# Performance work log

Hardware: AMD Instinct MI355X
Metric: run time of the kernel (lower is better)

The kernel has to match this reference:

```python
import jax, jax.numpy as jnp
from jax import lax
import numpy as np

DIM = 384
HEADS = 8
MLP_HIDDEN = int(DIM * 4.0)
EPS = 1e-5


def layer_norm(x, g, b):
    m = jnp.mean(x, axis=-1, keepdims=True)
    v = jnp.mean((x - m) ** 2, axis=-1, keepdims=True)
    return (x - m) * lax.rsqrt(v + EPS) * g + b


def conv_pos_enc(x, H, W, w, b):
    # x: (B, N, C) -> depthwise 3x3 conv residual, act=Identity (cpe_act=False)
    B, N, C = x.shape
    feat = jnp.transpose(x, (0, 2, 1)).reshape(B, C, H, W)
    feat = lax.conv_general_dilated(
        feat, w, window_strides=(1, 1), padding='SAME',
        feature_group_count=C, dimension_numbers=('NCHW', 'OIHW', 'NCHW'))
    feat = feat + b[None, :, None, None]
    feat = jnp.transpose(feat.reshape(B, C, N), (0, 2, 1))
    return x + feat


def channel_attn(x, qkv_w, proj_w, proj_b):
    B, N, C = x.shape
    h = HEADS
    hd = C // h
    scale = hd ** (-0.5)
    qkv = x @ qkv_w.T                                # (B, N, 3C)
    qkv = qkv.reshape(B, N, 3, h, hd)
    qkv = jnp.transpose(qkv, (2, 0, 3, 1, 4))        # (3, B, h, N, hd)
    q, k, v = qkv[0], qkv[1], qkv[2]
    k = k * scale
    attn = jnp.einsum('bhnd,bhne->bhde', k, v)       # (B, h, hd, hd)
    attn = jax.nn.softmax(attn, axis=-1)
    out = jnp.einsum('bhde,bhne->bhnd', attn, q)     # (B, h, N, hd)
    out = jnp.transpose(out, (0, 2, 1, 3)).reshape(B, N, C)
    return out @ proj_w.T + proj_b


def mlp(x, fc1_w, fc1_b, fc2_w, fc2_b):
    h = jax.nn.gelu(x @ fc1_w.T + fc1_b, approximate=False)
    return h @ fc2_w.T + fc2_b


def setup_inputs() -> dict:
    key = jax.random.key(0)
    ks = jax.random.split(key, 12)
    C, Hd = DIM, MLP_HIDDEN
    s = 0.02
    return {
        'x': jax.random.normal(ks[0], (32, 784, C), dtype=jnp.float32),
        'H': 28,
        'W': 28,
        'cpe0_w': jax.random.normal(ks[1], (C, 1, 3, 3), dtype=jnp.float32) * s,
        'cpe0_b': jnp.zeros((C,), dtype=jnp.float32),
        'cpe1_w': jax.random.normal(ks[2], (C, 1, 3, 3), dtype=jnp.float32) * s,
        'cpe1_b': jnp.zeros((C,), dtype=jnp.float32),
        'norm1_g': jnp.ones((C,), dtype=jnp.float32),
        'norm1_b': jnp.zeros((C,), dtype=jnp.float32),
        'qkv_w': jax.random.normal(ks[3], (3 * C, C), dtype=jnp.float32) * s,
        'proj_w': jax.random.normal(ks[4], (C, C), dtype=jnp.float32) * s,
        'proj_b': jnp.zeros((C,), dtype=jnp.float32),
        'norm2_g': jnp.ones((C,), dtype=jnp.float32),
        'norm2_b': jnp.zeros((C,), dtype=jnp.float32),
        'fc1_w': jax.random.normal(ks[5], (Hd, C), dtype=jnp.float32) * s,
        'fc1_b': jnp.zeros((Hd,), dtype=jnp.float32),
        'fc2_w': jax.random.normal(ks[6], (C, Hd), dtype=jnp.float32) * s,
        'fc2_b': jnp.zeros((C,), dtype=jnp.float32),
    }


def reference(x, H, W, cpe0_w, cpe0_b, cpe1_w, cpe1_b, norm1_g, norm1_b,
              qkv_w, proj_w, proj_b, norm2_g, norm2_b,
              fc1_w, fc1_b, fc2_w, fc2_b):
    x = conv_pos_enc(x, H, W, cpe0_w, cpe0_b)
    cur = layer_norm(x, norm1_g, norm1_b)
    x = x + channel_attn(cur, qkv_w, proj_w, proj_b)
    x = conv_pos_enc(x, H, W, cpe1_w, cpe1_b)
    x = x + mlp(layer_norm(x, norm2_g, norm2_b), fc1_w, fc1_b, fc2_w, fc2_b)
    return x
```

## Files before the change

kernel.cpp:

```cpp
#include <hip/hip_runtime.h>
#include <hip/hip_bf16.h>
#include <math.h>
#include <stdint.h>

#define B_     32
#define HH_    28
#define WW_    28
#define N_     784
#define C_     384
#define M_     25088
#define HEADS_ 8
#define HD_    48
#define HID_   1536

typedef __bf16 bf16;
typedef __attribute__((ext_vector_type(8))) __bf16 bf16x8;
typedef __attribute__((ext_vector_type(4))) __bf16 bf16x4;
typedef __attribute__((ext_vector_type(4))) float f32x4;

__device__ __forceinline__ void gload_lds16(const void* g, void* l) {
    __builtin_amdgcn_global_load_lds(
        (const __attribute__((address_space(1))) unsigned int*)g,
        (__attribute__((address_space(3))) unsigned int*)(uintptr_t)l,
        16, 0, 0);
}

__global__ void convert4_kernel(const float* __restrict__ a, int na,
                                const float* __restrict__ b, int nb,
                                const float* __restrict__ c, int nc,
                                const float* __restrict__ d, int nd,
                                bf16* __restrict__ out) {
    int i = blockIdx.x * 256 + threadIdx.x;
    int j = i;
    const float* src;
    if (j < na) src = a + j;
    else { j -= na;
        if (j < nb) src = b + j;
        else { j -= nb;
            if (j < nc) src = c + j;
            else { j -= nc;
                if (j >= nd) return;
                src = d + j; } } }
    out[i] = (bf16)(*src);
}

__global__ __launch_bounds__(384)
void cpe_ln_kernel(const float* __restrict__ x, const float* __restrict__ w,
                   const float* __restrict__ bias, float* __restrict__ y,
                   const float* __restrict__ g, const float* __restrict__ beta,
                   bf16* __restrict__ lnout) {
    __shared__ float red[4][96];
    const int t = threadIdx.x;
    const int tpos = t / 96;
    const int cg = t - tpos * 96;
    const int c4 = cg * 4;
    const int row = blockIdx.x * 4 + tpos;
    const int b = row / N_;
    const int n = row - b * N_;
    const int py = n / WW_, px = n - py * WW_;
    const float* wc = w + c4 * 9;

    float4 acc = *(const float4*)(bias + c4);
    float4 ctr = *(const float4*)(x + (size_t)row * C_ + c4);

    if (py >= 1 && py <= 26 && px >= 1 && px <= 26) {
        const float* p0 = x + (size_t)(row - WW_ - 1) * C_ + c4;
        const float* p1 = p0 + (size_t)WW_ * C_;
        const float* p2 = p1 + (size_t)WW_ * C_;
        float4 a0 = *(const float4*)(p0);
        float4 a1 = *(const float4*)(p0 + C_);
        float4 a2 = *(const float4*)(p0 + 2 * C_);
        float4 b0 = *(const float4*)(p1);
        float4 b2 = *(const float4*)(p1 + 2 * C_);
        float4 c0 = *(const float4*)(p2);
        float4 c1 = *(const float4*)(p2 + C_);
        float4 c2 = *(const float4*)(p2 + 2 * C_);
        float4 b1 = ctr;
        #define TAP(V, TI) \
            acc.x += wc[TI] * V.x; acc.y += wc[9 + TI] * V.y; \
            acc.z += wc[18 + TI] * V.z; acc.w += wc[27 + TI] * V.w;
        TAP(a0, 0) TAP(a1, 1) TAP(a2, 2)
        TAP(b0, 3) TAP(b1, 4) TAP(b2, 5)
        TAP(c0, 6) TAP(c1, 7) TAP(c2, 8)
        #undef TAP
    } else {
        #pragma unroll
        for (int ky = 0; ky < 3; ky++) {
            int yy = py + ky - 1;
            if (yy < 0 || yy >= HH_) continue;
            #pragma unroll
            for (int kx = 0; kx < 3; kx++) {
                int xx = px + kx - 1;
                if (xx < 0 || xx >= WW_) continue;
                int tap = ky * 3 + kx;
                float4 xv = (ky == 1 && kx == 1) ? ctr
                          : *(const float4*)(x + (size_t)(b * N_ + yy * WW_ + xx) * C_ + c4);
                acc.x += wc[tap] * xv.x;
                acc.y += wc[9 + tap] * xv.y;
                acc.z += wc[18 + tap] * xv.z;
                acc.w += wc[27 + tap] * xv.w;
            }
        }
    }
    acc.x += ctr.x; acc.y += ctr.y; acc.z += ctr.z; acc.w += ctr.w;
    *(float4*)(y + (size_t)row * C_ + c4) = acc;

    red[tpos][cg] = acc.x + acc.y + acc.z + acc.w;
    __syncthreads();
    #pragma unroll
    for (int s = 48; s >= 3; s >>= 1) {
        if (cg < s) red[tpos][cg] += red[tpos][cg + s];
        __syncthreads();
    }
    float mean = (red[tpos][0] + red[tpos][1] + red[tpos][2]) * (1.f / C_);
    __syncthreads();
    float dx = acc.x - mean, dy = acc.y - mean, dz = acc.z - mean, dw = acc.w - mean;
    red[tpos][cg] = dx * dx + dy * dy + dz * dz + dw * dw;
    __syncthreads();
    #pragma unroll
    for (int s = 48; s >= 3; s >>= 1) {
        if (cg < s) red[tpos][cg] += red[tpos][cg + s];
        __syncthreads();
    }
    float var = (red[tpos][0] + red[tpos][1] + red[tpos][2]) * (1.f / C_);
    float rstd = rsqrtf(var + 1e-5f);
    float4 gv = *(const float4*)(g + c4);
    float4 bv = *(const float4*)(beta + c4);
    bf16x4 ov;
    ov[0] = (bf16)(dx * rstd * gv.x + bv.x);
    ov[1] = (bf16)(dy * rstd * gv.y + bv.y);
    ov[2] = (bf16)(dz * rstd * gv.z + bv.z);
    ov[3] = (bf16)(dw * rstd * gv.w + bv.w);
    *(bf16x4*)(lnout + (size_t)row * C_ + c4) = ov;
}

template<bool BIAS, bool GELU, bool RESID, bool OUTBF>
__global__ __launch_bounds__(256)
void gemm_kernel(const bf16* __restrict__ A, const bf16* __restrict__ Wt,
                 const float* __restrict__ bias, const float* __restrict__ resid,
                 void* __restrict__ outp, int M, int N, int K) {
    __shared__ __align__(16) bf16 As[2 * 128 * 32];
    __shared__ __align__(16) bf16 Bs[2 * 128 * 32];
    const int bm = blockIdx.y * 128, bn = blockIdx.x * 128;
    const int t = threadIdx.x;
    const int wave = t >> 6, lane = t & 63;
    const int wm = (wave & 1) * 64, wn = (wave >> 1) * 64;
    const int quad = lane >> 4, r = lane & 15;

    const int ldrow = lane >> 2;
    const int ldcol = (lane & 3) * 8;
    const bf16* ga0 = A  + (size_t)(bm + wave * 32 + ldrow) * K + ldcol;
    const bf16* ga1 = ga0 + (size_t)16 * K;
    const bf16* gb0 = Wt + (size_t)(bn + wave * 32 + ldrow) * K + ldcol;
    const bf16* gb1 = gb0 + (size_t)16 * K;
    const int lbase = wave * 32 * 32;

    f32x4 acc[4][4] = {};

    gload_lds16(ga0, &As[lbase]);
    gload_lds16(ga1, &As[lbase + 512]);
    gload_lds16(gb0, &Bs[lbase]);
    gload_lds16(gb1, &Bs[lbase + 512]);

    int buf = 0;
    for (int k0 = 0; k0 < K; k0 += 32) {
        __syncthreads();
        if (k0 + 32 < K) {
            const int nb = (buf ^ 1) * 4096;
            gload_lds16(ga0 + k0 + 32, &As[nb + lbase]);
            gload_lds16(ga1 + k0 + 32, &As[nb + lbase + 512]);
            gload_lds16(gb0 + k0 + 32, &Bs[nb + lbase]);
            gload_lds16(gb1 + k0 + 32, &Bs[nb + lbase + 512]);
        }
        const bf16* as = &As[buf * 4096];
        const bf16* bs = &Bs[buf * 4096];
        bf16x8 af[4], bfr[4];
        #pragma unroll
        for (int i = 0; i < 4; i++)
            af[i] = *(const bf16x8*)(&as[(wm + i * 16 + r) * 32 + quad * 8]);
        #pragma unroll
        for (int j = 0; j < 4; j++)
            bfr[j] = *(const bf16x8*)(&bs[(wn + j * 16 + r) * 32 + quad * 8]);
        #pragma unroll
        for (int i = 0; i < 4; i++)
            #pragma unroll
            for (int j = 0; j < 4; j++)
                acc[i][j] = __builtin_amdgcn_mfma_f32_16x16x32_bf16(af[i], bfr[j], acc[i][j], 0, 0, 0);
        buf ^= 1;
    }

    #pragma unroll
    for (int i = 0; i < 4; i++) {
        #pragma unroll
        for (int j = 0; j < 4; j++) {
            int n = bn + wn + j * 16 + r;
            float bv = BIAS ? bias[n] : 0.f;
            #pragma unroll
            for (int e = 0; e < 4; e++) {
                int m = bm + wm + i * 16 + quad * 4 + e;
                float val = acc[i][j][e] + bv;
                if (GELU) val = 0.5f * val * (1.f + erff(val * 0.70710678118654752f));
                if (RESID) val += resid[(size_t)m * N + n];
                if (OUTBF) ((bf16*)outp)[(size_t)m * N + n] = (bf16)val;
                else       ((float*)outp)[(size_t)m * N + n] = val;
            }
        }
    }
}

__global__ __launch_bounds__(256)
void attn_fused_kernel(const bf16* __restrict__ qkvb, bf16* __restrict__ outp) {
    __shared__ __align__(16) bf16 stage[4][3872];
    __shared__ float Sred[4][48][49];
    __shared__ __align__(16) bf16 attn_s[48 * 72];

    const int bh = blockIdx.x;
    const int b = bh >> 3, h = bh & 7;
    const int t = threadIdx.x;
    const int wave = t >> 6, lane = t & 63;
    const int quad = lane >> 4, r = lane & 15;
    const int tensor = lane >> 5;
    const int n_local = lane & 31;

    const size_t qkv_base = (size_t)b * N_ * 1152;
    const int toff = 384 + tensor * 384 + h * 48;

    f32x4 acc[3][3] = {};
    bf16* kT = &stage[wave][0];
    bf16* vT = &stage[wave][1936];
    bf16* myT = &stage[wave][tensor * 1936];

    for (int c = wave; c < 25; c += 4) {
        int n0 = c * 32;
        bf16 rowbuf[48];
        if (n0 + n_local < N_) {
            const uint4* src = (const uint4*)(qkvb + qkv_base + (size_t)(n0 + n_local) * 1152 + toff);
            #pragma unroll
            for (int i = 0; i < 6; i++) *(uint4*)(&rowbuf[i * 8]) = src[i];
        } else {
            #pragma unroll
            for (int i = 0; i < 48; i++) rowbuf[i] = (bf16)0.f;
        }
        #pragma unroll
        for (int d = 0; d < 48; d++) myT[d * 40 + n_local] = rowbuf[d];
        bf16x8 af[3], bfv[3];
        #pragma unroll
        for (int i = 0; i < 3; i++) af[i]  = *(const bf16x8*)(&kT[(i * 16 + r) * 40 + quad * 8]);
        #pragma unroll
        for (int j = 0; j < 3; j++) bfv[j] = *(const bf16x8*)(&vT[(j * 16 + r) * 40 + quad * 8]);
        #pragma unroll
        for (int i = 0; i < 3; i++)
            #pragma unroll
            for (int j = 0; j < 3; j++)
                acc[i][j] = __builtin_amdgcn_mfma_f32_16x16x32_bf16(af[i], bfv[j], acc[i][j], 0, 0, 0);
    }

    #pragma unroll
    for (int i = 0; i < 3; i++)
        #pragma unroll
        for (int j = 0; j < 3; j++)
            #pragma unroll
            for (int e = 0; e < 4; e++)
                Sred[wave][i * 16 + quad * 4 + e][j * 16 + r] = acc[i][j][e];
    __syncthreads();

    if (t < 48) {
        float row[48];
        float mx = -1e30f;
        #pragma unroll
        for (int e = 0; e < 48; e++) {
            float s = Sred[0][t][e] + Sred[1][t][e] + Sred[2][t][e] + Sred[3][t][e];
            s *= 0.14433756729740644f;
            row[e] = s;
            mx = fmaxf(mx, s);
        }
        float sum = 0.f;
        #pragma unroll
        for (int e = 0; e < 48; e++) { float ex = __expf(row[e] - mx); row[e] = ex; sum += ex; }
        float inv = 1.f / sum;
        #pragma unroll
        for (int e = 0; e < 48; e++) attn_s[t * 72 + e] = (bf16)(row[e] * inv);
        #pragma unroll
        for (int e = 48; e < 64; e++) attn_s[t * 72 + e] = (bf16)0.f;
    }
    __syncthreads();

    const bf16* qbase = qkvb + qkv_base + h * 48;
    for (int nt = wave; nt < 49; nt += 4) {
        int n0 = nt * 16;
        f32x4 oacc[3] = {};
        #pragma unroll
        for (int kc = 0; kc < 2; kc++) {
            bf16x8 bq = *(const bf16x8*)(qbase + (size_t)(n0 + r) * 1152 + kc * 32 + quad * 8);
            #pragma unroll
            for (int i = 0; i < 3; i++) {
                bf16x8 aa = *(const bf16x8*)(&attn_s[(i * 16 + r) * 72 + kc * 32 + quad * 8]);
                oacc[i] = __builtin_amdgcn_mfma_f32_16x16x32_bf16(aa, bq, oacc[i], 0, 0, 0);
            }
        }
        #pragma unroll
        for (int i = 0; i < 3; i++) {
            bf16x4 ov;
            #pragma unroll
            for (int e = 0; e < 4; e++) ov[e] = (bf16)oacc[i][e];
            *(bf16x4*)(outp + (size_t)(b * N_ + n0 + r) * 384 + h * 48 + i * 16 + quad * 4) = ov;
        }
    }
}

extern "C" void kernel_launch(void* const* d_in, const int* in_sizes, int n_in,
                              void* d_out, int out_size, void* d_ws, size_t ws_size,
                              hipStream_t stream) {
    const float* x      = (const float*)d_in[0];
    const float* cpe0_w = (const float*)d_in[3];
    const float* cpe0_b = (const float*)d_in[4];
    const float* cpe1_w = (const float*)d_in[5];
    const float* cpe1_b = (const float*)d_in[6];
    const float* n1g    = (const float*)d_in[7];
    const float* n1b    = (const float*)d_in[8];
    const float* qkv_w  = (const float*)d_in[9];
    const float* proj_w = (const float*)d_in[10];
    const float* proj_b = (const float*)d_in[11];
    const float* n2g    = (const float*)d_in[12];
    const float* n2b    = (const float*)d_in[13];
    const float* fc1_w  = (const float*)d_in[14];
    const float* fc1_b  = (const float*)d_in[15];
    const float* fc2_w  = (const float*)d_in[16];
    const float* fc2_b  = (const float*)d_in[17];

    char* ws = (char*)d_ws;
    size_t off = 0;
    bf16* cur    = (bf16*)(ws + off); off += (size_t)M_ * C_ * 2;
    bf16* qkvb   = (bf16*)(ws + off);
    float* x3    = (float*)qkvb;
    off += (size_t)M_ * 1152 * 2;
    bf16* hbuf   = (bf16*)(ws + off); off += (size_t)M_ * HID_ * 2;
    bf16* qkv_wb  = (bf16*)(ws + off); off += (size_t)1152 * 384 * 2;
    bf16* proj_wb = (bf16*)(ws + off); off += (size_t)384 * 384 * 2;
    bf16* fc1_wb  = (bf16*)(ws + off); off += (size_t)HID_ * 384 * 2;
    bf16* fc2_wb  = (bf16*)(ws + off); off += (size_t)384 * HID_ * 2;
    float* out = (float*)d_out;

    const int na = 442368, nb = 147456, nc = 589824, nd = 589824;
    convert4_kernel<<<(na + nb + nc + nd + 255) / 256, 256, 0, stream>>>(
        qkv_w, na, proj_w, nb, fc1_w, nc, fc2_w, nd, qkv_wb);

    cpe_ln_kernel<<<M_ / 4, 384, 0, stream>>>(x, cpe0_w, cpe0_b, out, n1g, n1b, cur);
    gemm_kernel<false, false, false, true><<<dim3(1152 / 128, M_ / 128), 256, 0, stream>>>(
        cur, qkv_wb, nullptr, nullptr, qkvb, M_, 1152, 384);
    attn_fused_kernel<<<256, 256, 0, stream>>>(qkvb, cur);
    gemm_kernel<true, false, true, false><<<dim3(384 / 128, M_ / 128), 256, 0, stream>>>(
        cur, proj_wb, proj_b, out, out, M_, 384, 384);
    cpe_ln_kernel<<<M_ / 4, 384, 0, stream>>>(out, cpe1_w, cpe1_b, x3, n2g, n2b, cur);
    gemm_kernel<true, true, false, true><<<dim3(HID_ / 128, M_ / 128), 256, 0, stream>>>(
        cur, fc1_wb, fc1_b, nullptr, hbuf, M_, HID_, 384);
    gemm_kernel<true, false, true, false><<<dim3(384 / 128, M_ / 128), 256, 0, stream>>>(
        hbuf, fc2_wb, fc2_b, x3, out, M_, 384, HID_);
}
```

Before: 451.2 us.

## Triple-buffer GEMM LDS prefetch and add grouped block swizzle for L2 reuse

The bf16 MFMA GEMM moves from double-buffered to triple-buffered global-to-LDS loads. Tiles are prefetched two K-steps ahead, and a partial `s_waitcnt vmcnt(4)` replaces the full wait before each barrier, so memory latency overlaps more of the MFMA work. The block index is also remapped into groups of 8 row-tiles, so neighbouring blocks share A and W tiles in L2. The cost is 48KB of LDS per block instead of 32KB, which may lower occupancy, plus a peeled final iteration.

```diff
diff --git a/kernel.cpp b/kernel.cpp
--- a/kernel.cpp
+++ b/kernel.cpp
@@ -139,9 +139,17 @@
 void gemm_kernel(const bf16* __restrict__ A, const bf16* __restrict__ Wt,
                  const float* __restrict__ bias, const float* __restrict__ resid,
                  void* __restrict__ outp, int M, int N, int K) {
-    __shared__ __align__(16) bf16 As[2 * 128 * 32];
-    __shared__ __align__(16) bf16 Bs[2 * 128 * 32];
-    const int bm = blockIdx.y * 128, bn = blockIdx.x * 128;
+    __shared__ __align__(16) bf16 As[3 * 4096];
+    __shared__ __align__(16) bf16 Bs[3 * 4096];
+
+    const int nbn = gridDim.x, nbm = gridDim.y;
+    const int f = blockIdx.y * nbn + blockIdx.x;
+    const int grp = f / (8 * nbn);
+    const int rem = f - grp * 8 * nbn;
+    const int rows = min(8, nbm - grp * 8);
+    const int bm = (grp * 8 + rem % rows) * 128;
+    const int bn = (rem / rows) * 128;
+
     const int t = threadIdx.x;
     const int wave = t >> 6, lane = t & 63;
     const int wm = (wave & 1) * 64, wn = (wave >> 1) * 64;
@@ -161,16 +169,22 @@
     gload_lds16(ga1, &As[lbase + 512]);
     gload_lds16(gb0, &Bs[lbase]);
     gload_lds16(gb1, &Bs[lbase + 512]);
+    gload_lds16(ga0 + 32, &As[4096 + lbase]);
+    gload_lds16(ga1 + 32, &As[4096 + lbase + 512]);
+    gload_lds16(gb0 + 32, &Bs[4096 + lbase]);
+    gload_lds16(gb1 + 32, &Bs[4096 + lbase + 512]);
 
     int buf = 0;
-    for (int k0 = 0; k0 < K; k0 += 32) {
-        __syncthreads();
-        if (k0 + 32 < K) {
-            const int nb = (buf ^ 1) * 4096;
-            gload_lds16(ga0 + k0 + 32, &As[nb + lbase]);
-            gload_lds16(ga1 + k0 + 32, &As[nb + lbase + 512]);
-            gload_lds16(gb0 + k0 + 32, &Bs[nb + lbase]);
-            gload_lds16(gb1 + k0 + 32, &Bs[nb + lbase + 512]);
+    int k0 = 0;
+    for (; k0 < K - 32; k0 += 32) {
+        asm volatile("s_waitcnt vmcnt(4)" ::: "memory");
+        asm volatile("s_barrier" ::: "memory");
+        if (k0 + 64 < K) {
+            const int nb3 = (buf == 0 ? 2 : buf - 1) * 4096;
+            gload_lds16(ga0 + k0 + 64, &As[nb3 + lbase]);
+            gload_lds16(ga1 + k0 + 64, &As[nb3 + lbase + 512]);
+            gload_lds16(gb0 + k0 + 64, &Bs[nb3 + lbase]);
+            gload_lds16(gb1 + k0 + 64, &Bs[nb3 + lbase + 512]);
         }
         const bf16* as = &As[buf * 4096];
         const bf16* bs = &Bs[buf * 4096];
@@ -186,7 +200,25 @@
             #pragma unroll
             for (int j = 0; j < 4; j++)
                 acc[i][j] = __builtin_amdgcn_mfma_f32_16x16x32_bf16(af[i], bfr[j], acc[i][j], 0, 0, 0);
-        buf ^= 1;
+        buf = (buf == 2) ? 0 : buf + 1;
+    }
+    {
+        asm volatile("s_waitcnt vmcnt(0)" ::: "memory");
+        asm volatile("s_barrier" ::: "memory");
+        const bf16* as = &As[buf * 4096];
+        const bf16* bs = &Bs[buf * 4096];
+        bf16x8 af[4], bfr[4];
+        #pragma unroll
+        for (int i = 0; i < 4; i++)
+            af[i] = *(const bf16x8*)(&as[(wm + i * 16 + r) * 32 + quad * 8]);
+        #pragma unroll
+        for (int j = 0; j < 4; j++)
+            bfr[j] = *(const bf16x8*)(&bs[(wn + j * 16 + r) * 32 + quad * 8]);
+        #pragma unroll
+        for (int i = 0; i < 4; i++)
+            #pragma unroll
+            for (int j = 0; j < 4; j++)
+                acc[i][j] = __builtin_amdgcn_mfma_f32_16x16x32_bf16(af[i], bfr[j], acc[i][j], 0, 0, 0);
     }
 
     #pragma unroll
```

New measurement: 419.9 us. -7.0%, faster.
